# Kernel tuning notes

Hardware: AMD Instinct MI355X
Metric: run time of the kernel (lower is better)

## Reference

```python
import jax, jax.numpy as jnp
import numpy as np

B, T, HID = 2, 2048, 2048
NH = 8
D = HID // NH  # head_dim = 256 (expand_ratio=1 so input_dim == hidden_size)
EPS_RMS = 1e-8   # RMSNorm inside BitLinear
EPS_LN = 1e-5    # layernorm_eps for g_norm


def _rms(x, w, eps):
    # weighted RMSNorm over last dim
    return x * jax.lax.rsqrt(jnp.mean(x * x, axis=-1, keepdims=True) + eps) * w


def _act_quant(x):
    # per-token 8-bit fake quant with straight-through estimator
    s = 127.0 / jnp.clip(jnp.max(jnp.abs(x), axis=-1, keepdims=True), 1e-5)
    q = jnp.clip(jnp.round(x * s), -128, 127) / s
    return x + jax.lax.stop_gradient(q - x)


def _weight_quant(w):
    # ternary weight quantization (BitNet b1.58) with STE
    s = 1.0 / jnp.clip(jnp.mean(jnp.abs(w)), 1e-5)
    q = jnp.clip(jnp.round(w * s), -1, 1) / s
    return w + jax.lax.stop_gradient(q - w)


def _bitlinear(x, w, norm_w):
    # FusedBitLinear: RMSNorm -> activation quant -> ternary-weight linear
    xq = _act_quant(_rms(x, norm_w, EPS_RMS))
    return jnp.einsum('btk,ok->bto', xq, _weight_quant(w))


def setup_inputs() -> dict:
    key = jax.random.key(0)
    ks = jax.random.split(key, 5)
    std = 2 ** (-2.5) * np.sqrt(2.0 / (HID + HID))  # xavier_uniform-ish std with gain 2^-2.5
    return {
        'hidden_states': jax.random.normal(ks[0], (B, T, HID), dtype=jnp.float32),
        'w_i': jax.random.normal(ks[1], (HID, HID), dtype=jnp.float32) * std,
        'w_f': jax.random.normal(ks[2], (HID, HID), dtype=jnp.float32) * std,
        'w_g': jax.random.normal(ks[3], (HID, HID), dtype=jnp.float32) * std,
        'w_o': jax.random.normal(ks[4], (HID, HID), dtype=jnp.float32) * std,
        'n_i': jnp.ones((HID,), jnp.float32),
        'n_f': jnp.ones((HID,), jnp.float32),
        'n_g': jnp.ones((HID,), jnp.float32),
        'n_o': jnp.ones((HID,), jnp.float32),
        'gn_w': jnp.ones((HID,), jnp.float32),
    }


def reference(hidden_states, w_i, w_f, w_g, w_o, n_i, n_f, n_g, n_o, gn_w):
    hs = hidden_states
    i = _bitlinear(hs, w_i, n_i)                      # [B,T,HID]
    f = jax.nn.sigmoid(_bitlinear(hs, w_f, n_f))      # forget gate
    # swiglu(i, 1 - f) = silu(i) * (1 - f)
    i = i * jax.nn.sigmoid(i) * (1.0 - f)

    # b l (h d) -> t b h d for scan
    def to_tbhd(x):
        return x.reshape(B, T, NH, D).transpose(1, 0, 2, 3)

    i_t, f_t = to_tbhd(i), to_tbhd(f)

    def step(h, ft_it):
        ft, it = ft_it
        h = ft * h + it
        return h, h

    h0 = jnp.zeros((B, NH, D), dtype=i.dtype)
    _, o = jax.lax.scan(step, h0, (f_t, i_t))         # [T,B,NH,D]
    o = o.transpose(1, 0, 2, 3).reshape(B, T, HID)     # b l (h d)

    # g_norm(g_proj(hs), o): rmsnorm(g) * o * sigmoid(o)
    g = _bitlinear(hs, w_g, n_g)
    o = _rms(g, gn_w, EPS_LN) * o * jax.nn.sigmoid(o)
    return _bitlinear(o, w_o, n_o)
```

## Files before the change

kernel.cpp:

```cpp
#include <hip/hip_runtime.h>
#include <math.h>

#define HID 2048
#define TOKENS 4096
#define TT 2048
#define NCH 4096
#define NC 32
#define CL 64
#define WELEM 4194304

typedef unsigned short u16;
typedef signed char i8;
typedef int i32x4 __attribute__((ext_vector_type(4)));

__device__ inline float sigm(float x) { return 1.0f / (1.0f + expf(-x)); }
__device__ inline u16 f2bf_rn(float v) {
  unsigned b = __float_as_uint(v);
  unsigned r = b + 0x7FFFu + ((b >> 16) & 1u);
  return (u16)(r >> 16);
}
__device__ inline float bf2f(u16 h) {
  return __uint_as_float((unsigned)h << 16);
}

__device__ inline float wred_sum(float v) {
#pragma unroll
  for (int o = 32; o > 0; o >>= 1) v += __shfl_down(v, o);
  return v;
}
__device__ inline float wred_max(float v) {
#pragma unroll
  for (int o = 32; o > 0; o >>= 1) v = fmaxf(v, __shfl_down(v, o));
  return v;
}
__device__ inline double wred_sumd(double v) {
#pragma unroll
  for (int o = 32; o > 0; o >>= 1) v += __shfl_down(v, o);
  return v;
}

__device__ __forceinline__ void gl_lds16(const void* g, void* l) {
  __builtin_amdgcn_global_load_lds(
      (__attribute__((address_space(1))) void*)(void*)g,
      (__attribute__((address_space(3))) void*)l, 16, 0, 0);
}

__device__ __forceinline__ int pack8(const int* qi) {
  return (qi[0] & 255) | ((qi[1] & 255) << 8) | ((qi[2] & 255) << 16)
       | ((qi[3] & 255) << 24);
}

__global__ __launch_bounds__(256) void absmean_kernel(
    const float* __restrict__ w0, const float* __restrict__ w1,
    const float* __restrict__ w2, const float* __restrict__ w3,
    double* __restrict__ wsum) {
  int widx = blockIdx.x >> 9;
  int blk = blockIdx.x & 511;
  const float* w = widx == 0 ? w0 : widx == 1 ? w1 : widx == 2 ? w2 : w3;
  size_t base = (size_t)blk * 8192;
  double acc = 0.0;
#pragma unroll
  for (int r = 0; r < 8; ++r) {
    float4 v = *(const float4*)&w[base + (size_t)(r * 256 + threadIdx.x) * 4];
    acc += (double)fabsf(v.x) + (double)fabsf(v.y) + (double)fabsf(v.z) +
           (double)fabsf(v.w);
  }
  acc = wred_sumd(acc);
  __shared__ double sh[4];
  int tid = threadIdx.x;
  if ((tid & 63) == 0) sh[tid >> 6] = acc;
  __syncthreads();
  if (tid == 0) atomicAdd(&wsum[widx], (sh[0] + sh[1]) + (sh[2] + sh[3]));
}

__global__ __launch_bounds__(256) void prep_kernel(
    const float* __restrict__ w0, const float* __restrict__ w1,
    const float* __restrict__ w2, const float* __restrict__ w3,
    const double* __restrict__ wsum, i8* __restrict__ q0, i8* __restrict__ q1,
    i8* __restrict__ q2, i8* __restrict__ q3, const float* __restrict__ X,
    const float* __restrict__ nw0, const float* __restrict__ nw1,
    const float* __restrict__ nw2, i8* __restrict__ Xq0, i8* __restrict__ Xq1,
    i8* __restrict__ Xq2, float* __restrict__ inv0, float* __restrict__ inv1,
    float* __restrict__ inv2) {
  if (blockIdx.x < 8192) {
    int sel = blockIdx.x >> 11;
    int blk = blockIdx.x & 2047;
    const float* w = sel == 0 ? w0 : sel == 1 ? w1 : sel == 2 ? w2 : w3;
    i8* wq = sel == 0 ? q0 : sel == 1 ? q1 : sel == 2 ? q2 : q3;
    int widx = sel == 0 ? 1 : sel == 1 ? 0 : sel;
    double mean = wsum[widx] * (1.0 / (double)WELEM);
    float s = (float)(1.0 / fmax(mean, 1e-5));
    size_t base = (size_t)blk * 2048 + (size_t)threadIdx.x * 8;
    float4 va = *(const float4*)&w[base];
    float4 vb = *(const float4*)&w[base + 4];
    float vv[8] = {va.x, va.y, va.z, va.w, vb.x, vb.y, vb.z, vb.w};
    int qi[8];
#pragma unroll
    for (int j = 0; j < 8; ++j) {
      float q1v = rintf(vv[j] * s);
      q1v = fminf(fmaxf(q1v, -1.0f), 1.0f);
      qi[j] = (int)q1v;
    }
    *(int2*)&wq[base] = make_int2(pack8(qi), pack8(qi + 4));
    return;
  }
  int tok = blockIdx.x - 8192;
  int tid = threadIdx.x;
  const float* xrow = X + (size_t)tok * HID;
  int c0 = tid * 8;
  float x[8];
  *(float4*)&x[0] = *(const float4*)&xrow[c0];
  *(float4*)&x[4] = *(const float4*)&xrow[c0 + 4];
  float ss = 0.0f;
#pragma unroll
  for (int j = 0; j < 8; ++j) ss += x[j] * x[j];
  __shared__ float sh[4];
  float v = wred_sum(ss);
  if ((tid & 63) == 0) sh[tid >> 6] = v;
  __syncthreads();
  float tot = (sh[0] + sh[1]) + (sh[2] + sh[3]);
  float rstd = (float)(1.0 / sqrt((double)(tot * (1.0f / HID)) + 1e-8));
#pragma unroll
  for (int pass = 0; pass < 3; ++pass) {
    const float* nw = pass == 0 ? nw0 : pass == 1 ? nw1 : nw2;
    i8* Xq = pass == 0 ? Xq0 : pass == 1 ? Xq1 : Xq2;
    float* inv_s = pass == 0 ? inv0 : pass == 1 ? inv1 : inv2;
    float y[8];
    float amax = 0.0f;
#pragma unroll
    for (int j = 0; j < 8; ++j) {
      y[j] = x[j] * rstd * nw[c0 + j];
      amax = fmaxf(amax, fabsf(y[j]));
    }
    __syncthreads();
    float vv = wred_max(amax);
    if ((tid & 63) == 0) sh[tid >> 6] = vv;
    __syncthreads();
    float am = fmaxf(fmaxf(fmaxf(sh[0], sh[1]), fmaxf(sh[2], sh[3])), 1e-5f);
    float s = 127.0f / am;
    int qi[8];
#pragma unroll
    for (int j = 0; j < 8; ++j) {
      float qq = rintf(y[j] * s);
      qq = fminf(fmaxf(qq, -128.0f), 127.0f);
      qi[j] = (int)qq;
    }
    *(int2*)&Xq[(size_t)tok * HID + c0] = make_int2(pack8(qi), pack8(qi + 4));
    if (tid == 0) inv_s[tok] = am * (1.0f / 127.0f);
  }
}

template <int NSEG, bool F32OUT>
__global__ __launch_bounds__(512, 4) void gemm8_kernel(
    const i8* __restrict__ A0, const i8* __restrict__ A1,
    const i8* __restrict__ A2, const i8* __restrict__ W0,
    const i8* __restrict__ W1, const i8* __restrict__ W2,
    const float* __restrict__ inv0, const float* __restrict__ inv1,
    const float* __restrict__ inv2, const double* __restrict__ wsum,
    int widx0, int widx1, int widx2, void* __restrict__ O0,
    void* __restrict__ O1, void* __restrict__ O2) {
  const int tid = threadIdx.x;
  const int cpx = gridDim.x >> 3;
  const int lid = blockIdx.x;
  const int swz = (lid & 7) * cpx + (lid >> 3);
  const int seg = NSEG == 1 ? 0 : (swz >> 8);
  const int idx = swz & 255;
  const int n0 = (idx & 7) * 256;
  const int m0 = (idx >> 3) * 128;

  const i8* Aq = seg == 0 ? A0 : seg == 1 ? A1 : A2;
  const i8* Wq = seg == 0 ? W0 : seg == 1 ? W1 : W2;
  const float* inv_s = seg == 0 ? inv0 : seg == 1 ? inv1 : inv2;
  void* Out = seg == 0 ? O0 : seg == 1 ? O1 : O2;
  const int widx = seg == 0 ? widx0 : seg == 1 ? widx1 : widx2;

  __shared__ __align__(16) i8 As[2][8192];
  __shared__ __align__(16) i8 Bs[2][16384];
  float wscale = (float)fmax(wsum[widx] * (1.0 / (double)WELEM), 1e-5);

  const int wave = tid >> 6, lane = tid & 63;
  const int wm = wave >> 2;
  const int wn = wave & 3;
  const int lrow = lane & 15;
  const int ksel = lane >> 4;
  const int phys = ((ksel ^ ((lrow >> 1) & 3)) << 4);
  const int srl = lane >> 2;
  const int sg = (lane >> 3) & 3;
  const int skoff = ((lane & 3) ^ sg) << 4;

  const i8* Ab = Aq + (size_t)m0 * HID;
  const i8* Wb = Wq + (size_t)n0 * HID;

  i32x4 acc[4][4];
#pragma unroll
  for (int i = 0; i < 4; ++i)
#pragma unroll
    for (int j = 0; j < 4; ++j)
#pragma unroll
      for (int r = 0; r < 4; ++r) acc[i][j][r] = 0;

#define STAGE(buf, k0)                                                        \
  {                                                                           \
    int rowA = wave * 16 + srl;                                               \
    gl_lds16(&Ab[(size_t)rowA * HID + (k0) + skoff], &As[buf][wave * 1024]);  \
    int rowB0 = wave * 32 + srl;                                              \
    gl_lds16(&Wb[(size_t)rowB0 * HID + (k0) + skoff], &Bs[buf][wave * 2048]); \
    int rowB1 = wave * 32 + 16 + srl;                                         \
    gl_lds16(&Wb[(size_t)rowB1 * HID + (k0) + skoff],                         \
             &Bs[buf][wave * 2048 + 1024]);                                   \
  }

  const int NT = HID / 64;
  STAGE(0, 0)
  __syncthreads();
  int cur = 0;
  for (int kt = 0; kt < NT; ++kt) {
    if (kt + 1 < NT) STAGE(cur ^ 1, (kt + 1) * 64)
    i32x4 af[4], bfr[4];
#pragma unroll
    for (int i = 0; i < 4; ++i) {
      int ra = wm * 64 + i * 16 + lrow;
      af[i] = *(const i32x4*)&As[cur][ra * 64 + phys];
    }
#pragma unroll
    for (int j = 0; j < 4; ++j) {
      int rb = wn * 64 + j * 16 + lrow;
      bfr[j] = *(const i32x4*)&Bs[cur][rb * 64 + phys];
    }
    __builtin_amdgcn_s_setprio(1);
#pragma unroll
    for (int i = 0; i < 4; ++i)
#pragma unroll
      for (int j = 0; j < 4; ++j)
        acc[i][j] = __builtin_amdgcn_mfma_i32_16x16x64_i8(af[i], bfr[j],
                                                          acc[i][j], 0, 0, 0);
    __builtin_amdgcn_s_setprio(0);
    __syncthreads();
    cur ^= 1;
  }
#undef STAGE

#pragma unroll
  for (int i = 0; i < 4; ++i) {
    int rbase = m0 + wm * 64 + i * 16 + (lane >> 4) * 4;
#pragma unroll
    for (int j = 0; j < 4; ++j) {
      int col = n0 + wn * 64 + j * 16 + lrow;
#pragma unroll
      for (int r = 0; r < 4; ++r) {
        int row = rbase + r;
        float v = (float)acc[i][j][r] * inv_s[row] * wscale;
        float rr;
        if (NSEG == 3)
          rr = seg == 0 ? sigm(v) : seg == 1 ? v * sigm(v) : v;
        else
          rr = v;
        size_t oidx = (size_t)row * HID + col;
        if (F32OUT)
          ((float*)Out)[oidx] = rr;
        else
          ((u16*)Out)[oidx] = f2bf_rn(rr);
      }
    }
  }
}

__global__ __launch_bounds__(256) void scan1_kernel(
    const u16* __restrict__ F, u16* __restrict__ IO, float* __restrict__ P,
    float* __restrict__ H) {
  int c = blockIdx.x * 256 + threadIdx.x;
  int q = blockIdx.y;
  size_t base =
      (size_t)(c >> 11) * TT * HID + (c & 2047) + (size_t)q * CL * HID;
  float h = 0.0f, p = 1.0f;
#pragma unroll 4
  for (int t = 0; t < CL; ++t) {
    size_t idx = base + (size_t)t * HID;
    float f = bf2f(F[idx]);
    float iv = bf2f(IO[idx]);
    h = fmaf(f, h, iv - iv * f);
    p *= f;
    IO[idx] = f2bf_rn(h);
  }
  P[q * NCH + c] = p;
  H[q * NCH + c] = h;
}

__global__ __launch_bounds__(256) void scan23_kernel(
    const u16* __restrict__ F, const float* __restrict__ P,
    const float* __restrict__ H, u16* __restrict__ IO) {
  int c = blockIdx.x * 256 + threadIdx.x;
  int q = blockIdx.y + 1;
  float carry = 0.0f;
  for (int qq = 0; qq < q; ++qq)
    carry = fmaf(P[qq * NCH + c], carry, H[qq * NCH + c]);
  if (carry == 0.0f) return;
  size_t base =
      (size_t)(c >> 11) * TT * HID + (c & 2047) + (size_t)q * CL * HID;
  float p = 1.0f;
#pragma unroll 4
  for (int t = 0; t < CL; ++t) {
    size_t idx = base + (size_t)t * HID;
    p *= bf2f(F[idx]);
    IO[idx] = f2bf_rn(fmaf(p, carry, bf2f(IO[idx])));
  }
}

__global__ __launch_bounds__(256) void combine_quant_kernel(
    const u16* __restrict__ G, const float* __restrict__ gnw,
    const u16* __restrict__ O, const float* __restrict__ nw,
    i8* __restrict__ Xq, float* __restrict__ inv_s) {
  int tok = blockIdx.x;
  int tid = threadIdx.x;
  int c0 = tid * 8;
  const u16* grow = G + (size_t)tok * HID;
  const u16* orow = O + (size_t)tok * HID;
  ushort4 ga = *(const ushort4*)&grow[c0];
  ushort4 gb = *(const ushort4*)&grow[c0 + 4];
  ushort4 oa = *(const ushort4*)&orow[c0];
  ushort4 ob = *(const ushort4*)&orow[c0 + 4];
  float g[8] = {bf2f(ga.x), bf2f(ga.y), bf2f(ga.z), bf2f(ga.w),
                bf2f(gb.x), bf2f(gb.y), bf2f(gb.z), bf2f(gb.w)};
  float o[8] = {bf2f(oa.x), bf2f(oa.y), bf2f(oa.z), bf2f(oa.w),
                bf2f(ob.x), bf2f(ob.y), bf2f(ob.z), bf2f(ob.w)};
  __shared__ float sh[4];
  float ss = 0.0f;
#pragma unroll
  for (int j = 0; j < 8; ++j) ss += g[j] * g[j];
  float v = wred_sum(ss);
  if ((tid & 63) == 0) sh[tid >> 6] = v;
  __syncthreads();
  float tot = (sh[0] + sh[1]) + (sh[2] + sh[3]);
  float rstd_g = (float)(1.0 / sqrt((double)(tot * (1.0f / HID)) + 1e-5));
  float on[8];
  float ss2 = 0.0f;
#pragma unroll
  for (int j = 0; j < 8; ++j) {
    on[j] = g[j] * rstd_g * gnw[c0 + j] * o[j] * sigm(o[j]);
    ss2 += on[j] * on[j];
  }
  __syncthreads();
  v = wred_sum(ss2);
  if ((tid & 63) == 0) sh[tid >> 6] = v;
  __syncthreads();
  float tot2 = (sh[0] + sh[1]) + (sh[2] + sh[3]);
  float rstd_o = (float)(1.0 / sqrt((double)(tot2 * (1.0f / HID)) + 1e-8));
  float y[8];
  float amax = 0.0f;
#pragma unroll
  for (int j = 0; j < 8; ++j) {
    y[j] = on[j] * rstd_o * nw[c0 + j];
    amax = fmaxf(amax, fabsf(y[j]));
  }
  __syncthreads();
  v = wred_max(amax);
  if ((tid & 63) == 0) sh[tid >> 6] = v;
  __syncthreads();
  float am = fmaxf(fmaxf(fmaxf(sh[0], sh[1]), fmaxf(sh[2], sh[3])), 1e-5f);
  float s = 127.0f / am;
  int qi[8];
#pragma unroll
  for (int j = 0; j < 8; ++j) {
    float qq = rintf(y[j] * s);
    qq = fminf(fmaxf(qq, -128.0f), 127.0f);
    qi[j] = (int)qq;
  }
  *(int2*)&Xq[(size_t)tok * HID + c0] = make_int2(pack8(qi), pack8(qi + 4));
  if (tid == 0) inv_s[tok] = am * (1.0f / 127.0f);
}

extern "C" void kernel_launch(void* const* d_in, const int* in_sizes, int n_in,
                              void* d_out, int out_size, void* d_ws,
                              size_t ws_size, hipStream_t stream) {
  const float* hs = (const float*)d_in[0];
  const float* w_i = (const float*)d_in[1];
  const float* w_f = (const float*)d_in[2];
  const float* w_g = (const float*)d_in[3];
  const float* w_o = (const float*)d_in[4];
  const float* n_i = (const float*)d_in[5];
  const float* n_f = (const float*)d_in[6];
  const float* n_g = (const float*)d_in[7];
  const float* n_o = (const float*)d_in[8];
  const float* gn_w = (const float*)d_in[9];
  float* Out = (float*)d_out;

  char* ws = (char*)d_ws;
  i8* WQ0 = (i8*)ws;
  i8* WQ1 = (i8*)(ws + 4194304);
  i8* WQ2 = (i8*)(ws + 8388608);
  i8* WQ3 = (i8*)(ws + 12582912);
  i8* XQ0 = (i8*)(ws + 16777216);
  i8* XQ1 = (i8*)(ws + 25165824);
  i8* XQ2 = (i8*)(ws + 33554432);
  u16* F = (u16*)(ws + 41943040);
  u16* OB = (u16*)(ws + 58720256);
  u16* G = (u16*)(ws + 75497472);
  float* invs0 = (float*)(ws + 92274688);
  float* invs1 = (float*)(ws + 92291072);
  float* invs2 = (float*)(ws + 92307456);
  double* wsum = (double*)(ws + 92323840);
  float* scanP = (float*)(ws + 92324864);
  float* scanH = (float*)(ws + 92849152);

  hipMemsetAsync(wsum, 0, 4 * sizeof(double), stream);
  absmean_kernel<<<2048, 256, 0, stream>>>(w_i, w_f, w_g, w_o, wsum);

  prep_kernel<<<12288, 256, 0, stream>>>(w_f, w_i, w_g, w_o, wsum, WQ0, WQ1,
                                         WQ2, WQ3, hs, n_f, n_i, n_g, XQ0,
                                         XQ1, XQ2, invs0, invs1, invs2);

  gemm8_kernel<3, false><<<768, 512, 0, stream>>>(
      XQ0, XQ1, XQ2, WQ0, WQ1, WQ2, invs0, invs1, invs2, wsum, 1, 0, 2, F, OB,
      G);

  scan1_kernel<<<dim3(NCH / 256, NC), 256, 0, stream>>>(F, OB, scanP, scanH);
  scan23_kernel<<<dim3(NCH / 256, NC - 1), 256, 0, stream>>>(F, scanP, scanH,
                                                             OB);

  combine_quant_kernel<<<TOKENS, 256, 0, stream>>>(G, gn_w, OB, n_o, XQ0,
                                                   invs0);

  gemm8_kernel<1, true><<<256, 512, 0, stream>>>(
      XQ0, XQ0, XQ0, WQ3, WQ3, WQ3, invs0, invs0, invs0, wsum, 3, 3, 3, Out,
      Out, Out);
}
```

Before: 217.6 us.

## Deepen int8 GEMM pipeline to a 4-slot LDS ring with explicit vmcnt waits

Replaces the double-buffered int8 MFMA GEMM main loop with a 4-slot shared-memory ring that prefetches three K-tiles ahead. It uses explicit s_waitcnt vmcnt counts and a single barrier per iteration. The global-to-LDS loads for future tiles are split into two parts and interleaved between two halves of the MFMA work, with A-fragment reads also split. The goal is to hide global-load latency better, but it quadruples LDS per block (about 96 KB), which lowers the number of blocks that fit per CU. The launch bound is relaxed to match.

```diff
diff --git a/kernel.cpp b/kernel.cpp
--- a/kernel.cpp
+++ b/kernel.cpp
@@ -151,7 +151,7 @@
 }
 
 template <int NSEG, bool F32OUT>
-__global__ __launch_bounds__(512, 4) void gemm8_kernel(
+__global__ __launch_bounds__(512, 2) void gemm256_kernel(
     const i8* __restrict__ A0, const i8* __restrict__ A1,
     const i8* __restrict__ A2, const i8* __restrict__ W0,
     const i8* __restrict__ W1, const i8* __restrict__ W2,
@@ -174,8 +174,8 @@
   void* Out = seg == 0 ? O0 : seg == 1 ? O1 : O2;
   const int widx = seg == 0 ? widx0 : seg == 1 ? widx1 : widx2;
 
-  __shared__ __align__(16) i8 As[2][8192];
-  __shared__ __align__(16) i8 Bs[2][16384];
+  __shared__ __align__(16) i8 Apl[4][8192];
+  __shared__ __align__(16) i8 Bpl[4][16384];
   float wscale = (float)fmax(wsum[widx] * (1.0 / (double)WELEM), 1e-5);
 
   const int wave = tid >> 6, lane = tid & 63;
@@ -183,10 +183,9 @@
   const int wn = wave & 3;
   const int lrow = lane & 15;
   const int ksel = lane >> 4;
-  const int phys = ((ksel ^ ((lrow >> 1) & 3)) << 4);
-  const int srl = lane >> 2;
-  const int sg = (lane >> 3) & 3;
-  const int skoff = ((lane & 3) ^ sg) << 4;
+  const int rdcol = ((ksel ^ ((lrow >> 1) & 3)) << 4);
+  const int srow = lane >> 2;
+  const int scol = (((lane & 3) ^ ((lane >> 3) & 3)) << 4);
 
   const i8* Ab = Aq + (size_t)m0 * HID;
   const i8* Wb = Wq + (size_t)n0 * HID;
@@ -199,57 +198,76 @@
 #pragma unroll
       for (int r = 0; r < 4; ++r) acc[i][j][r] = 0;
 
-#define STAGE(buf, k0)                                                        \
-  {                                                                           \
-    int rowA = wave * 16 + srl;                                               \
-    gl_lds16(&Ab[(size_t)rowA * HID + (k0) + skoff], &As[buf][wave * 1024]);  \
-    int rowB0 = wave * 32 + srl;                                              \
-    gl_lds16(&Wb[(size_t)rowB0 * HID + (k0) + skoff], &Bs[buf][wave * 2048]); \
-    int rowB1 = wave * 32 + 16 + srl;                                         \
-    gl_lds16(&Wb[(size_t)rowB1 * HID + (k0) + skoff],                         \
-             &Bs[buf][wave * 2048 + 1024]);                                   \
-  }
-
-  const int NT = HID / 64;
-  STAGE(0, 0)
-  __syncthreads();
-  int cur = 0;
-  for (int kt = 0; kt < NT; ++kt) {
-    if (kt + 1 < NT) STAGE(cur ^ 1, (kt + 1) * 64)
-    i32x4 af[4], bfr[4];
-#pragma unroll
-    for (int i = 0; i < 4; ++i) {
-      int ra = wm * 64 + i * 16 + lrow;
-      af[i] = *(const i32x4*)&As[cur][ra * 64 + phys];
-    }
+#define STAGEU0(u_)                                                         \
+  {                                                                         \
+    int kb = ((u_) >> 1) * 128 + ((u_)&1) * 64;                             \
+    int sl = (u_)&3;                                                        \
+    gl_lds16(&Ab[(size_t)(wave * 16 + srow) * HID + kb + scol],             \
+             &Apl[sl][wave * 1024]);                                        \
+    gl_lds16(&Wb[(size_t)(wave * 32 + srow) * HID + kb + scol],             \
+             &Bpl[sl][wave * 2048]);                                        \
+  }
+#define STAGEU1(u_)                                                         \
+  {                                                                         \
+    int kb = ((u_) >> 1) * 128 + ((u_)&1) * 64;                             \
+    int sl = (u_)&3;                                                        \
+    gl_lds16(&Wb[(size_t)(wave * 32 + 16 + srow) * HID + kb + scol],        \
+             &Bpl[sl][wave * 2048 + 1024]);                                 \
+  }
+
+  STAGEU0(0) STAGEU1(0) STAGEU0(1) STAGEU1(1) STAGEU0(2) STAGEU1(2)
+
+  for (int u = 0; u < 32; ++u) {
+    if (u < 30)
+      asm volatile("s_waitcnt vmcnt(6)" ::: "memory");
+    else if (u == 30)
+      asm volatile("s_waitcnt vmcnt(3)" ::: "memory");
+    else
+      asm volatile("s_waitcnt vmcnt(0)" ::: "memory");
+    __builtin_amdgcn_s_barrier();
+    const int sl = u & 3;
+    i32x4 af0, af1, bf[4];
+    af0 = *(const i32x4*)&Apl[sl][(wm * 64 + 0 * 16 + lrow) * 64 + rdcol];
+    af1 = *(const i32x4*)&Apl[sl][(wm * 64 + 1 * 16 + lrow) * 64 + rdcol];
+#pragma unroll
+    for (int j = 0; j < 4; ++j)
+      bf[j] = *(const i32x4*)&Bpl[sl][(wn * 64 + j * 16 + lrow) * 64 + rdcol];
+    if (u < 29) STAGEU0(u + 3)
+    __builtin_amdgcn_s_setprio(1);
 #pragma unroll
     for (int j = 0; j < 4; ++j) {
-      int rb = wn * 64 + j * 16 + lrow;
-      bfr[j] = *(const i32x4*)&Bs[cur][rb * 64 + phys];
-    }
+      acc[0][j] = __builtin_amdgcn_mfma_i32_16x16x64_i8(af0, bf[j], acc[0][j],
+                                                        0, 0, 0);
+      acc[1][j] = __builtin_amdgcn_mfma_i32_16x16x64_i8(af1, bf[j], acc[1][j],
+                                                        0, 0, 0);
+    }
+    __builtin_amdgcn_s_setprio(0);
+    af0 = *(const i32x4*)&Apl[sl][(wm * 64 + 2 * 16 + lrow) * 64 + rdcol];
+    af1 = *(const i32x4*)&Apl[sl][(wm * 64 + 3 * 16 + lrow) * 64 + rdcol];
+    if (u < 29) STAGEU1(u + 3)
     __builtin_amdgcn_s_setprio(1);
 #pragma unroll
-    for (int i = 0; i < 4; ++i)
-#pragma unroll
-      for (int j = 0; j < 4; ++j)
-        acc[i][j] = __builtin_amdgcn_mfma_i32_16x16x64_i8(af[i], bfr[j],
-                                                          acc[i][j], 0, 0, 0);
+    for (int j = 0; j < 4; ++j) {
+      acc[2][j] = __builtin_amdgcn_mfma_i32_16x16x64_i8(af0, bf[j], acc[2][j],
+                                                        0, 0, 0);
+      acc[3][j] = __builtin_amdgcn_mfma_i32_16x16x64_i8(af1, bf[j], acc[3][j],
+                                                        0, 0, 0);
+    }
     __builtin_amdgcn_s_setprio(0);
-    __syncthreads();
-    cur ^= 1;
-  }
-#undef STAGE
-
-#pragma unroll
-  for (int i = 0; i < 4; ++i) {
-    int rbase = m0 + wm * 64 + i * 16 + (lane >> 4) * 4;
+  }
+#undef STAGEU0
+#undef STAGEU1
+
+#pragma unroll
+  for (int mi = 0; mi < 4; ++mi) {
+    int rbase = m0 + wm * 64 + mi * 16 + (lane >> 4) * 4;
 #pragma unroll
     for (int j = 0; j < 4; ++j) {
       int col = n0 + wn * 64 + j * 16 + lrow;
 #pragma unroll
       for (int r = 0; r < 4; ++r) {
         int row = rbase + r;
-        float v = (float)acc[i][j][r] * inv_s[row] * wscale;
+        float v = (float)acc[mi][j][r] * inv_s[row] * wscale;
         float rr;
         if (NSEG == 3)
           rr = seg == 0 ? sigm(v) : seg == 1 ? v * sigm(v) : v;
@@ -409,7 +427,7 @@
                                          WQ2, WQ3, hs, n_f, n_i, n_g, XQ0,
                                          XQ1, XQ2, invs0, invs1, invs2);
 
-  gemm8_kernel<3, false><<<768, 512, 0, stream>>>(
+  gemm256_kernel<3, false><<<768, 512, 0, stream>>>(
       XQ0, XQ1, XQ2, WQ0, WQ1, WQ2, invs0, invs1, invs2, wsum, 1, 0, 2, F, OB,
       G);
 
@@ -420,7 +438,7 @@
   combine_quant_kernel<<<TOKENS, 256, 0, stream>>>(G, gn_w, OB, n_o, XQ0,
                                                    invs0);
 
-  gemm8_kernel<1, true><<<256, 512, 0, stream>>>(
+  gemm256_kernel<1, true><<<256, 512, 0, stream>>>(
       XQ0, XQ0, XQ0, WQ3, WQ3, WQ3, invs0, invs0, invs0, wsum, 3, 3, 3, Out,
       Out, Out);
 }
```

Measured after the change: 225.1 us. 3.5% more time.
